# Kernel tuning notes

Measured on AMD Instinct MI355X. Metric: run time of the kernel, lower is better.

The kernel has to match this reference:

```python
import jax, jax.numpy as jnp
import numpy as np

# Fixed architecture constants (from DMGHAN.__init__ / Mamba defaults)
D_MODEL = 256; D_STATE = 16; D_CONV = 4; D_INNER = 512; DT_RANK = 16
EMBED = 1024; N_CLASSES = [5, 30, 80, 200, 600, 1500]
B, L = 8, 2048


def setup_inputs() -> dict:
    key = jax.random.key(0)
    ks = jax.random.split(key, 32)
    def p(i, shape, s=0.02):
        return jax.random.normal(ks[i], shape, jnp.float32) * s
    inp = {
        "x": jax.random.normal(ks[0], (B, L, EMBED), jnp.float32),
        # input_proj
        "W_proj": p(1, (D_MODEL, EMBED)), "b_proj": p(2, (D_MODEL,)),
        # Mamba block params
        "W_in": p(3, (2 * D_INNER, D_MODEL)),
        "conv_w": p(4, (D_INNER, 1, D_CONV), 0.1), "conv_b": p(5, (D_INNER,), 0.1),
        "W_xp": p(6, (DT_RANK + 2 * D_STATE, D_INNER)),
        "W_dt": p(7, (D_INNER, DT_RANK), 0.1), "b_dt": p(8, (D_INNER,), 0.1),
        "A_log": jnp.log(jnp.broadcast_to(jnp.arange(1., D_STATE + 1., dtype=jnp.float32), (D_INNER, D_STATE))),
        "Dp": jnp.ones((D_INNER,), jnp.float32),
        "W_out": p(9, (D_MODEL, D_INNER)),
        # 6 MultiheadAttention layers (in_proj packed [q;k;v], out_proj)
        "mha_in_w": p(10, (6, 3 * D_MODEL, D_MODEL)), "mha_in_b": p(11, (6, 3 * D_MODEL)),
        "mha_out_w": p(12, (6, D_MODEL, D_MODEL)), "mha_out_b": p(13, (6, D_MODEL)),
        # 5 gates: Linear(512, 256) + sigmoid
        "gate_w": p(14, (5, D_MODEL, 2 * D_MODEL)), "gate_b": p(15, (5, D_MODEL)),
    }
    for i, nc in enumerate(N_CLASSES):
        inp[f"Wc{i}"] = p(16 + i, (nc, D_MODEL))
        inp[f"bc{i}"] = p(22 + i, (nc,))
    return inp


def mamba_block(x, W_in, conv_w, conv_b, W_xp, W_dt, b_dt, A_log, Dp, W_out):
    # x: (B, L, D_MODEL)
    u, z = jnp.split(x @ W_in.T, 2, axis=-1)          # each (B, L, D_INNER)
    # causal depthwise conv over time
    uc = jax.lax.conv_general_dilated(
        u.transpose(0, 2, 1), conv_w, window_strides=(1,),
        padding=[(D_CONV - 1, 0)], dimension_numbers=('NCH', 'OIH', 'NCH'),
        feature_group_count=D_INNER)
    u = jax.nn.silu(uc.transpose(0, 2, 1) + conv_b)    # (B, L, D_INNER)
    xdbc = u @ W_xp.T                                  # (B, L, DT_RANK + 2*N)
    dt = jax.nn.softplus(xdbc[..., :DT_RANK] @ W_dt.T + b_dt)   # (B, L, D_INNER)
    Bm = xdbc[..., DT_RANK:DT_RANK + D_STATE]          # (B, L, N)
    Cm = xdbc[..., DT_RANK + D_STATE:]                 # (B, L, N)
    A = -jnp.exp(A_log)                                # (D_INNER, N)

    def step(h, inp):
        d_t, B_t, C_t, u_t = inp                       # (B,D_INNER),(B,N),(B,N),(B,D_INNER)
        h = jnp.exp(d_t[..., None] * A) * h + (d_t * u_t)[..., None] * B_t[:, None, :]
        y = jnp.einsum('bdn,bn->bd', h, C_t)
        return h, y

    h0 = jnp.zeros((x.shape[0], D_INNER, D_STATE), x.dtype)
    xs = (dt.transpose(1, 0, 2), Bm.transpose(1, 0, 2), Cm.transpose(1, 0, 2), u.transpose(1, 0, 2))
    _, ys = jax.lax.scan(step, h0, xs)                 # ys: (L, B, D_INNER)
    y = ys.transpose(1, 0, 2) + u * Dp
    y = y * jax.nn.silu(z)
    return y @ W_out.T                                 # (B, L, D_MODEL)


def reference(x, W_proj, b_proj, W_in, conv_w, conv_b, W_xp, W_dt, b_dt, A_log, Dp, W_out,
              mha_in_w, mha_in_b, mha_out_w, mha_out_b, gate_w, gate_b,
              Wc0, bc0, Wc1, bc1, Wc2, bc2, Wc3, bc3, Wc4, bc4, Wc5, bc5):
    h = x @ W_proj.T + b_proj                          # (B, L, 256)
    seq = mamba_block(h, W_in, conv_w, conv_b, W_xp, W_dt, b_dt, A_log, Dp, W_out)
    pooled = seq.mean(axis=1)                          # (B, 256)

    feats = []
    cur = None
    for i in range(6):
        if i == 0:
            f = pooled
        else:
            g = jax.nn.sigmoid(jnp.concatenate([cur, pooled], -1) @ gate_w[i - 1].T + gate_b[i - 1])
            f = g * cur + (1. - g) * pooled
        # MHA self-attention with seq_len=1: softmax over a single key is identically 1,
        # so attn_out = out_proj(v_proj(f)) exactly (same value AND gradients).
        v = f @ mha_in_w[i][2 * D_MODEL:].T + mha_in_b[i][2 * D_MODEL:]
        cur = v @ mha_out_w[i].T + mha_out_b[i]
        feats.append(cur)

    Wcs = [Wc0, Wc1, Wc2, Wc3, Wc4, Wc5]
    bcs = [bc0, bc1, bc2, bc3, bc4, bc5]
    return tuple(f @ W.T + b for f, W, b in zip(feats, Wcs, bcs))
```

## Files before the change

kernel.cpp:

```cpp
#include <hip/hip_runtime.h>
#include <stdint.h>

typedef unsigned short u16;
typedef uint32_t u32;
typedef __attribute__((ext_vector_type(8))) short bf16x8;
typedef __attribute__((ext_vector_type(4))) float f32x4;

__device__ __forceinline__ float bf2f(u16 u){ return __uint_as_float(((u32)u) << 16); }
__device__ __forceinline__ u16 f2bf(float f){
    u32 u = __float_as_uint(f);
    u += 0x7FFFu + ((u >> 16) & 1u);
    return (u16)(u >> 16);
}

#define AS1(p) ((const __attribute__((address_space(1))) void*)(p))
#define AS3(p) ((__attribute__((address_space(3))) void*)(p))

#define HW_GATE 0
#define HW_WVT  655360
#define HW_WO   1048576
#define HW_WOV  1441792
#define HW_TOT  1835008

#define NBLK 16
#define NC   64
#define CT   32

__global__ __launch_bounds__(256)
void convert_x(const float* __restrict__ xsrc, u16* __restrict__ dst)
{
    const int i = (blockIdx.x*256 + threadIdx.x)*8;
    const float4 a = *(const float4*)(xsrc + i);
    const float4 b = *(const float4*)(xsrc + i + 4);
    ushort4 o0; o0.x=f2bf(a.x); o0.y=f2bf(a.y); o0.z=f2bf(a.z); o0.w=f2bf(a.w);
    ushort4 o1; o1.x=f2bf(b.x); o1.y=f2bf(b.y); o1.z=f2bf(b.z); o1.w=f2bf(b.w);
    *(ushort4*)(dst+i) = o0; *(ushort4*)(dst+i+4) = o1;
}

__global__ __launch_bounds__(256)
void convert_w(const float* __restrict__ W_proj, const float* __restrict__ W_in,
               const float* __restrict__ W_xp,  const float* __restrict__ gate_w,
               const float* __restrict__ mha_in_w, const float* __restrict__ mha_out_w,
               u16* __restrict__ wproj, u16* __restrict__ win,
               u16* __restrict__ wxpp,  u16* __restrict__ whead,
               float* __restrict__ ysumG, unsigned* __restrict__ cnt)
{
    const int gid = blockIdx.x*256 + threadIdx.x;
    if(gid < 262144){
        wproj[gid] = f2bf(W_proj[gid]);
    } else if(gid < 786432){
        const int g = gid - 262144;
        win[g] = f2bf(W_in[g]);
    } else if(gid < 851968){
        const int g = gid - 786432;
        wxpp[g] = ((g >> 9) < 48) ? f2bf(W_xp[g]) : (u16)0;
    } else if(gid < 1507328){
        const int g = gid - 851968;
        whead[HW_GATE + g] = f2bf(gate_w[g]);
    } else if(gid < 1900544){
        const int g = gid - 1507328;
        const int i = g >> 16, k = (g >> 8) & 255, j = g & 255;
        whead[HW_WVT + g] = f2bf(mha_in_w[(size_t)i*196608 + 131072 + (size_t)j*256 + k]);
    } else if(gid < 2293760){
        const int g = gid - 1900544;
        whead[HW_WO + g] = f2bf(mha_out_w[g]);
    } else if(gid < 2297856){
        ysumG[gid - 2293760] = 0.f;
    } else if(gid < 2297920){
        cnt[gid - 2297856] = 0u;
    }
}

template<int EPI>
__global__ __launch_bounds__(256)
void gemm_bt(const u16* __restrict__ A, const u16* __restrict__ B,
             const float* __restrict__ bias, u16* __restrict__ C,
             int K, int lda, int ldb, int ldc, int nTilesN)
{
    __shared__ __align__(16) u16 As[128*32];
    __shared__ __align__(16) u16 Bs[128*32];
    const int tid  = threadIdx.x;
    const int nwg  = gridDim.x;
    const int bid0 = blockIdx.x;
    const int bid  = ((nwg & 7) == 0) ? (bid0 & 7)*(nwg >> 3) + (bid0 >> 3) : bid0;
    const int bm   = bid / nTilesN, bn = bid % nTilesN;
    const int m0   = bm*128, n0 = bn*128;
    const int lane = tid & 63, wave = tid >> 6;
    const int r1 = tid >> 2,        p1 = tid & 3;
    const int r2 = (tid+256) >> 2,  p2 = (tid+256) & 3;
    const u16* gA1 = A + (size_t)(m0 + r1)*lda + p1*8;
    const u16* gA2 = A + (size_t)(m0 + r2)*lda + p2*8;
    const u16* gB1 = B + (size_t)(n0 + r1)*ldb + p1*8;
    const u16* gB2 = B + (size_t)(n0 + r2)*ldb + p2*8;
    u16* lA1 = As + wave*512;
    u16* lA2 = As + 2048 + wave*512;
    u16* lB1 = Bs + wave*512;
    u16* lB2 = Bs + 2048 + wave*512;

    f32x4 acc[4][4];
    #pragma unroll
    for(int i=0;i<4;i++)
        #pragma unroll
        for(int j=0;j<4;j++) acc[i][j] = (f32x4){0.f,0.f,0.f,0.f};

    const int wm = (wave>>1)*64, wn = (wave&1)*64;
    const int fr = lane & 15, fq = lane >> 4;

    for(int k0 = 0; k0 < K; k0 += 32){
        __syncthreads();
        __builtin_amdgcn_global_load_lds(AS1(gA1 + k0), AS3(lA1), 16, 0, 0);
        __builtin_amdgcn_global_load_lds(AS1(gA2 + k0), AS3(lA2), 16, 0, 0);
        __builtin_amdgcn_global_load_lds(AS1(gB1 + k0), AS3(lB1), 16, 0, 0);
        __builtin_amdgcn_global_load_lds(AS1(gB2 + k0), AS3(lB2), 16, 0, 0);
        __syncthreads();
        bf16x8 af[4], bw[4];
        #pragma unroll
        for(int i=0;i<4;i++){
            af[i] = *(const bf16x8*)(As + (wm + 16*i + fr)*32 + fq*8);
            bw[i] = *(const bf16x8*)(Bs + (wn + 16*i + fr)*32 + fq*8);
        }
        #pragma unroll
        for(int i=0;i<4;i++)
            #pragma unroll
            for(int j=0;j<4;j++)
                acc[i][j] = __builtin_amdgcn_mfma_f32_16x16x32_bf16(af[i], bw[j], acc[i][j], 0,0,0);
    }

    const int mbase = m0 + wm + fq*4;
    #pragma unroll
    for(int j=0;j<4;j++){
        const int ncol = n0 + wn + 16*j + fr;
        const float bv = (EPI >= 1) ? bias[ncol] : 0.f;
        #pragma unroll
        for(int i=0;i<4;i++){
            #pragma unroll
            for(int r=0;r<4;r++){
                C[(size_t)(mbase + 16*i + r)*ldc + ncol] = f2bf(acc[i][j][r] + bv);
            }
        }
    }
}

__global__ __launch_bounds__(256)
void wov_k(u16* __restrict__ whead)
{
    __shared__ __align__(16) u16 As[128*32];
    __shared__ __align__(16) u16 Bs[128*32];
    const int tid  = threadIdx.x;
    const int st   = blockIdx.x >> 2;
    const int tile = blockIdx.x & 3;
    const int m0   = (tile>>1)*128, n0 = (tile&1)*128;
    const u16* A = whead + HW_WO  + (size_t)st*65536;
    const u16* B = whead + HW_WVT + (size_t)st*65536;
    u16*       C = whead + HW_WOV + (size_t)st*65536;
    const int lane = tid & 63, wave = tid >> 6;
    const int r1 = tid >> 2,        p1 = tid & 3;
    const int r2 = (tid+256) >> 2,  p2 = (tid+256) & 3;
    const u16* gA1 = A + (size_t)(m0 + r1)*256 + p1*8;
    const u16* gA2 = A + (size_t)(m0 + r2)*256 + p2*8;
    const u16* gB1 = B + (size_t)(n0 + r1)*256 + p1*8;
    const u16* gB2 = B + (size_t)(n0 + r2)*256 + p2*8;
    u16* lA1 = As + wave*512;
    u16* lA2 = As + 2048 + wave*512;
    u16* lB1 = Bs + wave*512;
    u16* lB2 = Bs + 2048 + wave*512;

    f32x4 acc[4][4];
    #pragma unroll
    for(int i=0;i<4;i++)
        #pragma unroll
        for(int j=0;j<4;j++) acc[i][j] = (f32x4){0.f,0.f,0.f,0.f};

    const int wm = (wave>>1)*64, wn = (wave&1)*64;
    const int fr = lane & 15, fq = lane >> 4;

    for(int k0 = 0; k0 < 256; k0 += 32){
        __syncthreads();
        __builtin_amdgcn_global_load_lds(AS1(gA1 + k0), AS3(lA1), 16, 0, 0);
        __builtin_amdgcn_global_load_lds(AS1(gA2 + k0), AS3(lA2), 16, 0, 0);
        __builtin_amdgcn_global_load_lds(AS1(gB1 + k0), AS3(lB1), 16, 0, 0);
        __builtin_amdgcn_global_load_lds(AS1(gB2 + k0), AS3(lB2), 16, 0, 0);
        __syncthreads();
        bf16x8 af[4], bw[4];
        #pragma unroll
        for(int i=0;i<4;i++){
            af[i] = *(const bf16x8*)(As + (wm + 16*i + fr)*32 + fq*8);
            bw[i] = *(const bf16x8*)(Bs + (wn + 16*i + fr)*32 + fq*8);
        }
        #pragma unroll
        for(int i=0;i<4;i++)
            #pragma unroll
            for(int j=0;j<4;j++)
                acc[i][j] = __builtin_amdgcn_mfma_f32_16x16x32_bf16(af[i], bw[j], acc[i][j], 0,0,0);
    }

    const int mbase = m0 + wm + fq*4;
    #pragma unroll
    for(int j=0;j<4;j++){
        const int ncol = n0 + wn + 16*j + fr;
        #pragma unroll
        for(int i=0;i<4;i++){
            #pragma unroll
            for(int r=0;r<4;r++){
                C[(size_t)(mbase + 16*i + r)*256 + ncol] = f2bf(acc[i][j][r]);
            }
        }
    }
}

__global__ __launch_bounds__(256)
void bcomb_k(const float* __restrict__ mha_out_w, const float* __restrict__ mha_in_b,
             const float* __restrict__ mha_out_b, float* __restrict__ bcomb)
{
    const int st = blockIdx.x, n = threadIdx.x;
    __shared__ float bv[256];
    bv[n] = mha_in_b[st*768 + 512 + n];
    __syncthreads();
    const float* w = mha_out_w + (size_t)st*65536 + (size_t)n*256;
    float s = mha_out_b[st*256 + n];
    for(int k=0;k<256;k++) s += w[k]*bv[k];
    bcomb[st*256 + n] = s;
}

__global__ __launch_bounds__(256)
void dt_kernel(const u16* __restrict__ xdbc, const float* __restrict__ W_dt,
               const float* __restrict__ b_dt, u16* __restrict__ dtb)
{
    const int m0 = blockIdx.x*64;
    const int d0 = threadIdx.x;
    float w0[16], w1[16];
    #pragma unroll
    for(int k=0;k<16;k++){ w0[k]=W_dt[d0*16+k]; w1[k]=W_dt[(d0+256)*16+k]; }
    const float bb0=b_dt[d0], bb1=b_dt[d0+256];
    for(int r=0;r<64;r++){
        const int m=m0+r;
        const bf16x8 v0 = *(const bf16x8*)(xdbc + (size_t)m*128);
        const bf16x8 v1 = *(const bf16x8*)(xdbc + (size_t)m*128 + 8);
        float a0=bb0, a1=bb1;
        #pragma unroll
        for(int k=0;k<8;k++){ const float xv=bf2f((u16)v0[k]); a0+=xv*w0[k]; a1+=xv*w1[k]; }
        #pragma unroll
        for(int k=0;k<8;k++){ const float xv=bf2f((u16)v1[k]); a0+=xv*w0[k+8]; a1+=xv*w1[k+8]; }
        a0 = (a0>15.f)? a0 : __logf(1.f+__expf(a0));
        a1 = (a1>15.f)? a1 : __logf(1.f+__expf(a1));
        dtb[(size_t)m*512+d0]     = f2bf(a0);
        dtb[(size_t)m*512+d0+256] = f2bf(a1);
    }
}

__global__ __launch_bounds__(256)
void conv_silu(const u16* __restrict__ xin, const float* __restrict__ conv_w,
               const float* __restrict__ conv_b, u16* __restrict__ u2)
{
    const int idx = blockIdx.x*256 + threadIdx.x;
    const int d = idx & 511;
    const int m = idx >> 9;
    const int l = m & 2047;
    const u16* base = xin + (size_t)m*1024 + d;
    float acc = conv_b[d];
    const float w0 = conv_w[d*4+0];
    const float w1 = conv_w[d*4+1];
    const float w2 = conv_w[d*4+2];
    const float w3 = conv_w[d*4+3];
    if(l >= 3) acc += bf2f(base[-3*1024])*w0;
    if(l >= 2) acc += bf2f(base[-2*1024])*w1;
    if(l >= 1) acc += bf2f(base[-1*1024])*w2;
    acc += bf2f(base[0])*w3;
    u2[idx] = f2bf(acc / (1.f + __expf(-acc)));
}

__global__ __launch_bounds__(512)
void scan_a(const u16* __restrict__ dtb, const u16* __restrict__ u2,
            const u16* __restrict__ xdbc,
            float* __restrict__ dts_out, float* __restrict__ S)
{
    const int b = blockIdx.x >> 6, c = blockIdx.x & 63;
    const int d = threadIdx.x;
    const int m0 = b*2048 + c*CT;
    __shared__ float Bsh[CT][16];
    {
        const int tt = d >> 4, n = d & 15;
        Bsh[tt][n] = bf2f(xdbc[(size_t)(m0+tt)*128 + 16 + n]);
    }
    __syncthreads();
    float h[16];
    #pragma unroll
    for(int n=0;n<16;n++) h[n] = 0.f;
    float dts = 0.f;
    for(int tb=0; tb<CT; tb+=8){
        float dtv[8], uv[8];
        #pragma unroll
        for(int q=0;q<8;q++){
            const size_t m = (size_t)(m0+tb+q)*512 + d;
            dtv[q] = bf2f(dtb[m]);
            uv[q]  = bf2f(u2[m]);
        }
        #pragma unroll
        for(int q=0;q<8;q++){
            const float du = dtv[q]*uv[q];
            dts += dtv[q];
            const float r = __expf(-dtv[q]);
            float p = 1.f;
            #pragma unroll
            for(int n=0;n<16;n++){
                p *= r;
                h[n] = p*h[n] + du*Bsh[tb+q][n];
            }
        }
    }
    const size_t o = (size_t)(b*NC + c)*512 + d;
    dts_out[o] = dts;
    #pragma unroll
    for(int n=0;n<16;n++) S[o*16 + n] = h[n];
}

__global__ __launch_bounds__(256)
void scan_b(const float* __restrict__ dts, float* __restrict__ S )
{
    const int gid = blockIdx.x*256 + threadIdx.x;
    const int b = gid >> 13;
    const int dn = gid & 8191;
    const int d = dn >> 4;
    const float nf = (float)((dn & 15) + 1);
    float h = 0.f;
    for(int c=0;c<NC;c++){
        const size_t od = (size_t)(b*NC + c)*512 + d;
        const float pn = __expf(-nf * dts[od]);
        const size_t o = od*16 + (dn & 15);
        const float s = S[o];
        S[o] = h;
        h = pn*h + s;
    }
}

__global__ __launch_bounds__(512)
void scan_c(const u16* __restrict__ dtb, const u16* __restrict__ u2,
            const u16* __restrict__ xdbc, const u16* __restrict__ xin,
            const float* __restrict__ Dp, const float* __restrict__ Hin,
            float* __restrict__ ysumG)
{
    const int b = blockIdx.x >> 6, c = blockIdx.x & 63;
    const int d = threadIdx.x;
    const int m0 = b*2048 + c*CT;
    __shared__ float Bsh[CT][16];
    __shared__ float Csh[CT][16];
    {
        const int tt = d >> 4, n = d & 15;
        const size_t row = (size_t)(m0+tt)*128;
        Bsh[tt][n] = bf2f(xdbc[row + 16 + n]);
        Csh[tt][n] = bf2f(xdbc[row + 32 + n]);
    }
    __syncthreads();
    const float Dpd = Dp[d];
    const size_t ho = ((size_t)(b*NC + c)*512 + d)*16;
    float h[16];
    #pragma unroll
    for(int n=0;n<16;n++) h[n] = Hin[ho+n];
    float ysum = 0.f;
    for(int tb=0; tb<CT; tb+=8){
        float dtv[8], uv[8], zv[8];
        #pragma unroll
        for(int q=0;q<8;q++){
            const size_t m = (size_t)(m0+tb+q)*512 + d;
            dtv[q] = bf2f(dtb[m]);
            uv[q]  = bf2f(u2[m]);
            zv[q]  = bf2f(xin[(size_t)(m0+tb+q)*1024 + 512 + d]);
        }
        #pragma unroll
        for(int q=0;q<8;q++){
            const float du = dtv[q]*uv[q];
            const float r = __expf(-dtv[q]);
            float p = 1.f;
            float y = 0.f;
            #pragma unroll
            for(int n=0;n<16;n++){
                p *= r;
                h[n] = p*h[n] + du*Bsh[tb+q][n];
                y += h[n]*Csh[tb+q][n];
            }
            y += uv[q]*Dpd;
            y *= zv[q] / (1.f + __expf(-zv[q]));
            ysum += y;
        }
    }
    atomicAdd(&ysumG[b*512 + d], ysum);
}

__device__ __forceinline__ void gridbar(unsigned* cnt, int ep)
{
    __syncthreads();
    if(threadIdx.x == 0){
        __threadfence();
        __hip_atomic_fetch_add(cnt, 1u, __ATOMIC_RELEASE, __HIP_MEMORY_SCOPE_AGENT);
        const unsigned tgt = (unsigned)(NBLK*ep);
        while(__hip_atomic_load(cnt, __ATOMIC_RELAXED, __HIP_MEMORY_SCOPE_AGENT) < tgt)
            __builtin_amdgcn_s_sleep(2);
        __threadfence();
    }
    __syncthreads();
}

__global__ __launch_bounds__(256)
void head_coop(const float* __restrict__ ysumG, const float* __restrict__ W_out,
               const u16* __restrict__ whead, const float* __restrict__ bcomb,
               const float* __restrict__ gate_b,
               u16* __restrict__ plA, u16* __restrict__ clA, u16* __restrict__ vA,
               float* __restrict__ feats, unsigned* cnt)
{
    __shared__ float pscr[2048];
    __shared__ float plL[128], clL[128];
    __shared__ float PgL[768];
    const int tid  = threadIdx.x;
    const int nb0  = blockIdx.x*16;
    const int lane = tid & 63, wave = tid >> 6;
    const int fr = lane & 15, fq = lane >> 4;
    const int nn = nb0 + fr;
    int ep = 0;

    {
        const int col16 = tid >> 4, seg = tid & 15;
        float part[8];
        #pragma unroll
        for(int b=0;b<8;b++) part[b] = 0.f;
        const float* wrow = W_out + (size_t)(nb0 + col16)*512 + seg*32;
        const float* ys   = ysumG + seg*32;
        for(int dd=0; dd<32; dd++){
            const float w = wrow[dd];
            #pragma unroll
            for(int b=0;b<8;b++) part[b] += ys[b*512 + dd]*w;
        }
        #pragma unroll
        for(int b=0;b<8;b++) pscr[(seg*16 + col16)*8 + b] = part[b];
        __syncthreads();
        if(tid < 128){
            const int b = tid & 7, c16 = tid >> 3;
            float s = 0.f;
            for(int g=0; g<16; g++) s += pscr[(g*16 + c16)*8 + b];
            s *= (1.f/2048.f);
            plL[b*16 + c16] = s;
            plA[b*256 + nb0 + c16] = f2bf(s);
        } else {
            const int idx = tid - 128, r = 8 + (idx >> 4), c = idx & 15;
            const int off = r*256 + nb0 + c;
            plA[off] = 0; clA[off] = 0; vA[off] = 0;
        }
    }
    gridbar(cnt, ++ep);

    if(wave == 0){
        bf16x8 af[8];
        #pragma unroll
        for(int i=0;i<8;i++) af[i] = *(const bf16x8*)(plA + fr*256 + i*32 + fq*8);
        {
            const u16* wb = whead + HW_WOV + (size_t)nn*256 + fq*8;
            bf16x8 bw[8];
            #pragma unroll
            for(int i=0;i<8;i++) bw[i] = *(const bf16x8*)(wb + i*32);
            f32x4 acc = (f32x4){0.f,0.f,0.f,0.f};
            #pragma unroll
            for(int i=0;i<8;i++)
                acc = __builtin_amdgcn_mfma_f32_16x16x32_bf16(af[i], bw[i], acc, 0,0,0);
            const float bc = bcomb[nn];
            #pragma unroll
            for(int r=0;r<4;r++){
                const int bi = fq*4 + r;
                if(bi < 8){
                    const float cv = acc[r] + bc;
                    clL[bi*16 + fr] = cv;
                    clA[bi*256 + nn] = f2bf(cv);
                    feats[bi*256 + nn] = cv;
                }
            }
        }
        #pragma unroll
        for(int st=1; st<6; st++){
            const u16* wb = whead + HW_GATE + (size_t)(st-1)*131072
                          + (size_t)nn*512 + 256 + fq*8;
            bf16x8 bw[8];
            #pragma unroll
            for(int i=0;i<8;i++) bw[i] = *(const bf16x8*)(wb + i*32);
            f32x4 acc = (f32x4){0.f,0.f,0.f,0.f};
            #pragma unroll
            for(int i=0;i<8;i++)
                acc = __builtin_amdgcn_mfma_f32_16x16x32_bf16(af[i], bw[i], acc, 0,0,0);
            const float gb = gate_b[(st-1)*256 + nn];
            #pragma unroll
            for(int r=0;r<4;r++){
                const int bi = fq*4 + r;
                if(bi < 8) PgL[st*128 + bi*16 + fr] = acc[r] + gb;
            }
        }
    }
    gridbar(cnt, ++ep);

    for(int st=1; st<6; st++){
        if(wave == 0){
            const u16* wb = whead + HW_GATE + (size_t)(st-1)*131072
                          + (size_t)nn*512 + fq*8;
            bf16x8 af[8], bw[8];
            #pragma unroll
            for(int i=0;i<8;i++) bw[i] = *(const bf16x8*)(wb + i*32);
            #pragma unroll
            for(int i=0;i<8;i++) af[i] = *(const bf16x8*)(clA + fr*256 + i*32 + fq*8);
            f32x4 acc = (f32x4){0.f,0.f,0.f,0.f};
            #pragma unroll
            for(int i=0;i<8;i++)
                acc = __builtin_amdgcn_mfma_f32_16x16x32_bf16(af[i], bw[i], acc, 0,0,0);
            #pragma unroll
            for(int r=0;r<4;r++){
                const int bi = fq*4 + r;
                if(bi < 8){
                    const float t = acc[r] + PgL[st*128 + bi*16 + fr];
                    const float g = 1.f/(1.f + __expf(-t));
                    const float f = g*clL[bi*16 + fr] + (1.f - g)*plL[bi*16 + fr];
                    vA[bi*256 + nn] = f2bf(f);
                }
            }
        }
        gridbar(cnt, ++ep);
        if(wave == 0){
            const u16* wb = whead + HW_WOV + (size_t)st*65536 + (size_t)nn*256 + fq*8;
            bf16x8 af[8], bw[8];
            #pragma unroll
            for(int i=0;i<8;i++) bw[i] = *(const bf16x8*)(wb + i*32);
            #pragma unroll
            for(int i=0;i<8;i++) af[i] = *(const bf16x8*)(vA + fr*256 + i*32 + fq*8);
            f32x4 acc = (f32x4){0.f,0.f,0.f,0.f};
            #pragma unroll
            for(int i=0;i<8;i++)
                acc = __builtin_amdgcn_mfma_f32_16x16x32_bf16(af[i], bw[i], acc, 0,0,0);
            const float bc = bcomb[st*256 + nn];
            #pragma unroll
            for(int r=0;r<4;r++){
                const int bi = fq*4 + r;
                if(bi < 8){
                    const float cv = acc[r] + bc;
                    clL[bi*16 + fr] = cv;
                    clA[bi*256 + nn] = f2bf(cv);
                    feats[(size_t)st*2048 + bi*256 + nn] = cv;
                }
            }
        }
        if(st < 5) gridbar(cnt, ++ep);
    }
}

__global__ __launch_bounds__(256)
void classifier_k(const float* __restrict__ feats,
    const float* __restrict__ W0, const float* __restrict__ b0,
    const float* __restrict__ W1, const float* __restrict__ b1,
    const float* __restrict__ W2, const float* __restrict__ b2,
    const float* __restrict__ W3, const float* __restrict__ b3,
    const float* __restrict__ W4, const float* __restrict__ b4,
    const float* __restrict__ W5, const float* __restrict__ b5,
    float* __restrict__ out)
{
    const int tid = blockIdx.x*256 + threadIdx.x;
    if(tid >= 19320) return;
    const int b  = tid & 7;
    const int ic = tid >> 3;
    int i, c, nc, ooff;
    const float *W, *bb;
    if(ic < 5)       { i=0; c=ic;      nc=5;    ooff=0;    W=W0; bb=b0; }
    else if(ic<35)   { i=1; c=ic-5;    nc=30;   ooff=40;   W=W1; bb=b1; }
    else if(ic<115)  { i=2; c=ic-35;   nc=80;   ooff=280;  W=W2; bb=b2; }
    else if(ic<315)  { i=3; c=ic-115;  nc=200;  ooff=920;  W=W3; bb=b3; }
    else if(ic<915)  { i=4; c=ic-315;  nc=600;  ooff=2520; W=W4; bb=b4; }
    else             { i=5; c=ic-915;  nc=1500; ooff=7320; W=W5; bb=b5; }
    const float4* f4 = (const float4*)(feats + ((size_t)i*8 + b)*256);
    const float4* w4 = (const float4*)(W + (size_t)c*256);
    float acc = bb[c];
    #pragma unroll 8
    for(int m=0;m<64;m++){
        const float4 a = f4[m], w = w4[m];
        acc += a.x*w.x + a.y*w.y + a.z*w.z + a.w*w.w;
    }
    out[ooff + b*nc + c] = acc;
}

extern "C" void kernel_launch(void* const* d_in, const int* in_sizes, int n_in,
                              void* d_out, int out_size, void* d_ws, size_t ws_size,
                              hipStream_t stream)
{
    const float* x         = (const float*)d_in[0];
    const float* W_proj    = (const float*)d_in[1];
    const float* b_proj    = (const float*)d_in[2];
    const float* W_in      = (const float*)d_in[3];
    const float* conv_w    = (const float*)d_in[4];
    const float* conv_b    = (const float*)d_in[5];
    const float* W_xp      = (const float*)d_in[6];
    const float* W_dt      = (const float*)d_in[7];
    const float* b_dt      = (const float*)d_in[8];
    const float* Dp        = (const float*)d_in[10];
    const float* W_out     = (const float*)d_in[11];
    const float* mha_in_w  = (const float*)d_in[12];
    const float* mha_in_b  = (const float*)d_in[13];
    const float* mha_out_w = (const float*)d_in[14];
    const float* mha_out_b = (const float*)d_in[15];
    const float* gate_w    = (const float*)d_in[16];
    const float* gate_b    = (const float*)d_in[17];

    char* ws = (char*)d_ws;
    u16*   xbf    = (u16*)  (ws + 0);
    u16*   xin    = (u16*)  (ws + 0);
    u16*   h      = (u16*)  (ws + 33554432);
    float* dts    = (float*)(ws + 33554432);
    u16*   u2     = (u16*)  (ws + 41943040);
    u16*   xdbc   = (u16*)  (ws + 58720256);
    u16*   dtb    = (u16*)  (ws + 62914560);
    float* S      = (float*)(ws + 79691776);
    float* ysumG  = (float*)(ws + 96468992);
    unsigned* cnt = (unsigned*)(ws + 96468992 + 16384);
    u16*   plA    = (u16*)  (ws + 96468992 + 16640);
    u16*   clA    = (u16*)  (ws + 96468992 + 24832);
    u16*   vA     = (u16*)  (ws + 96468992 + 33024);
    float* feats  = (float*)(ws + 97001472);
    u16*   wproj  = (u16*)  (ws + 97058816);
    u16*   win    = (u16*)  (ws + 97583104);
    u16*   wxpp   = (u16*)  (ws + 98631680);
    u16*   whead  = (u16*)  (ws + 98762752);
    float* bcomb  = (float*)(ws + 102432768);

    convert_x<<<dim3(8192), 256, 0, stream>>>(x, xbf);
    convert_w<<<dim3(8977), 256, 0, stream>>>(W_proj, W_in, W_xp, gate_w,
                                              mha_in_w, mha_out_w,
                                              wproj, win, wxpp, whead,
                                              ysumG, cnt);
    wov_k<<<dim3(24), 256, 0, stream>>>(whead);
    bcomb_k<<<dim3(6), 256, 0, stream>>>(mha_out_w, mha_in_b, mha_out_b, bcomb);

    gemm_bt<1><<<dim3(128*2), 256, 0, stream>>>(xbf, wproj, b_proj, h,
        1024, 1024, 1024, 256, 2);
    gemm_bt<0><<<dim3(128*8), 256, 0, stream>>>(h, win, nullptr, xin,
        256, 256, 256, 1024, 8);
    conv_silu<<<dim3(32768), 256, 0, stream>>>(xin, conv_w, conv_b, u2);
    gemm_bt<0><<<dim3(128), 256, 0, stream>>>(u2, wxpp, nullptr, xdbc,
        512, 512, 512, 128, 1);
    dt_kernel<<<dim3(256), 256, 0, stream>>>(xdbc, W_dt, b_dt, dtb);

    scan_a<<<dim3(512), 512, 0, stream>>>(dtb, u2, xdbc, dts, S);
    scan_b<<<dim3(256), 256, 0, stream>>>(dts, S);
    scan_c<<<dim3(512), 512, 0, stream>>>(dtb, u2, xdbc, xin, Dp, S, ysumG);

    head_coop<<<dim3(NBLK), 256, 0, stream>>>(ysumG, W_out, whead, bcomb,
                                              gate_b, plA, clA, vA, feats, cnt);

    classifier_k<<<dim3(76), 256, 0, stream>>>(feats,
        (const float*)d_in[18], (const float*)d_in[19],
        (const float*)d_in[20], (const float*)d_in[21],
        (const float*)d_in[22], (const float*)d_in[23],
        (const float*)d_in[24], (const float*)d_in[25],
        (const float*)d_in[26], (const float*)d_in[27],
        (const float*)d_in[28], (const float*)d_in[29],
        (float*)d_out);
}
```

Measured before the change: 439.1 us.

## Fold gate weights into value/out projections to halve grid barriers in head

```diff
diff --git a/kernel.cpp b/kernel.cpp
--- a/kernel.cpp
+++ b/kernel.cpp
@@ -21,6 +21,7 @@
 #define HW_WO   1048576
 #define HW_WOV  1441792
 #define HW_TOT  1835008
+#define HW_WGV  HW_WVT
 
 #define NBLK 16
 #define NC   64
@@ -209,6 +210,144 @@
 }
 
 __global__ __launch_bounds__(256)
+void wovT_k(const u16* __restrict__ whead, u16* __restrict__ wovt)
+{
+    __shared__ __align__(16) u16 As[128*32];
+    __shared__ __align__(16) u16 Bs[128*32];
+    const int tid  = threadIdx.x;
+    const int st   = blockIdx.x >> 2;
+    const int tile = blockIdx.x & 3;
+    const int m0   = (tile>>1)*128, n0 = (tile&1)*128;
+    const u16* A = whead + HW_WVT + (size_t)st*65536;
+    const u16* B = whead + HW_WO  + (size_t)st*65536;
+    u16*       C = wovt + (size_t)st*65536;
+    const int lane = tid & 63, wave = tid >> 6;
+    const int r1 = tid >> 2,        p1 = tid & 3;
+    const int r2 = (tid+256) >> 2,  p2 = (tid+256) & 3;
+    const u16* gA1 = A + (size_t)(m0 + r1)*256 + p1*8;
+    const u16* gA2 = A + (size_t)(m0 + r2)*256 + p2*8;
+    const u16* gB1 = B + (size_t)(n0 + r1)*256 + p1*8;
+    const u16* gB2 = B + (size_t)(n0 + r2)*256 + p2*8;
+    u16* lA1 = As + wave*512;
+    u16* lA2 = As + 2048 + wave*512;
+    u16* lB1 = Bs + wave*512;
+    u16* lB2 = Bs + 2048 + wave*512;
+
+    f32x4 acc[4][4];
+    #pragma unroll
+    for(int i=0;i<4;i++)
+        #pragma unroll
+        for(int j=0;j<4;j++) acc[i][j] = (f32x4){0.f,0.f,0.f,0.f};
+
+    const int wm = (wave>>1)*64, wn = (wave&1)*64;
+    const int fr = lane & 15, fq = lane >> 4;
+
+    for(int k0 = 0; k0 < 256; k0 += 32){
+        __syncthreads();
+        __builtin_amdgcn_global_load_lds(AS1(gA1 + k0), AS3(lA1), 16, 0, 0);
+        __builtin_amdgcn_global_load_lds(AS1(gA2 + k0), AS3(lA2), 16, 0, 0);
+        __builtin_amdgcn_global_load_lds(AS1(gB1 + k0), AS3(lB1), 16, 0, 0);
+        __builtin_amdgcn_global_load_lds(AS1(gB2 + k0), AS3(lB2), 16, 0, 0);
+        __syncthreads();
+        bf16x8 af[4], bw[4];
+        #pragma unroll
+        for(int i=0;i<4;i++){
+            af[i] = *(const bf16x8*)(As + (wm + 16*i + fr)*32 + fq*8);
+            bw[i] = *(const bf16x8*)(Bs + (wn + 16*i + fr)*32 + fq*8);
+        }
+        #pragma unroll
+        for(int i=0;i<4;i++)
+            #pragma unroll
+            for(int j=0;j<4;j++)
+                acc[i][j] = __builtin_amdgcn_mfma_f32_16x16x32_bf16(af[i], bw[j], acc[i][j], 0,0,0);
+    }
+
+    const int mbase = m0 + wm + fq*4;
+    #pragma unroll
+    for(int j=0;j<4;j++){
+        const int ncol = n0 + wn + 16*j + fr;
+        #pragma unroll
+        for(int i=0;i<4;i++){
+            #pragma unroll
+            for(int r=0;r<4;r++){
+                C[(size_t)(mbase + 16*i + r)*256 + ncol] = f2bf(acc[i][j][r]);
+            }
+        }
+    }
+}
+
+__global__ __launch_bounds__(256)
+void wgv_k(u16* __restrict__ whead, const u16* __restrict__ wovt)
+{
+    __shared__ __align__(16) u16 As[128*32];
+    __shared__ __align__(16) u16 Bs[128*32];
+    const int tid  = threadIdx.x;
+    const int st1  = blockIdx.x >> 2;
+    const int tile = blockIdx.x & 3;
+    const int m0   = (tile>>1)*128, n0 = (tile&1)*128;
+    const u16* A = whead + HW_GATE + (size_t)st1*131072;
+    const u16* B = wovt + (size_t)st1*65536;
+    u16*       C = whead + HW_WGV + (size_t)st1*65536;
+    const int lane = tid & 63, wave = tid >> 6;
+    const int r1 = tid >> 2,        p1 = tid & 3;
+    const int r2 = (tid+256) >> 2,  p2 = (tid+256) & 3;
+    const u16* gA1 = A + (size_t)(m0 + r1)*512 + p1*8;
+    const u16* gA2 = A + (size_t)(m0 + r2)*512 + p2*8;
+    const u16* gB1 = B + (size_t)(n0 + r1)*256 + p1*8;
+    const u16* gB2 = B + (size_t)(n0 + r2)*256 + p2*8;
+    u16* lA1 = As + wave*512;
+    u16* lA2 = As + 2048 + wave*512;
+    u16* lB1 = Bs + wave*512;
+    u16* lB2 = Bs + 2048 + wave*512;
+
+    f32x4 acc[4][4];
+    #pragma unroll
+    for(int i=0;i<4;i++)
+        #pragma unroll
+        for(int j=0;j<4;j++) acc[i][j] = (f32x4){0.f,0.f,0.f,0.f};
+
+    const int wm = (wave>>1)*64, wn = (wave&1)*64;
+    const int fr = lane & 15, fq = lane >> 4;
+
+    for(int k0 = 0; k0 < 256; k0 += 32){
+        __syncthreads();
+        __builtin_amdgcn_global_load_lds(AS1(gA1 + k0), AS3(lA1), 16, 0, 0);
+        __builtin_amdgcn_global_load_lds(AS1(gA2 + k0), AS3(lA2), 16, 0, 0);
+        __builtin_amdgcn_global_load_lds(AS1(gB1 + k0), AS3(lB1), 16, 0, 0);
+        __builtin_amdgcn_global_load_lds(AS1(gB2 + k0), AS3(lB2), 16, 0, 0);
+        __syncthreads();
+        bf16x8 af[4], bw[4];
+        #pragma unroll
+        for(int i=0;i<4;i++){
+            af[i] = *(const bf16x8*)(As + (wm + 16*i + fr)*32 + fq*8);
+            bw[i] = *(const bf16x8*)(Bs + (wn + 16*i + fr)*32 + fq*8);
+        }
+        #pragma unroll
+        for(int i=0;i<4;i++)
+            #pragma unroll
+            for(int j=0;j<4;j++)
+                acc[i][j] = __builtin_amdgcn_mfma_f32_16x16x32_bf16(af[i], bw[j], acc[i][j], 0,0,0);
+    }
+
+    const int mbase = m0 + wm + fq*4;
+    #pragma unroll
+    for(int j=0;j<4;j++){
+        const int ncol = n0 + wn + 16*j + fr;
+        #pragma unroll
+        for(int i=0;i<4;i++){
+            #pragma unroll
+            for(int r=0;r<4;r++){
+                const int mrow = mbase + 16*i + r;
+                float v = acc[i][j][r];
+                if(st1 == 0)
+                    v += bf2f(whead[HW_GATE + (size_t)mrow*512 + 256 + ncol]);
+                C[(size_t)mrow*256 + ncol] = f2bf(v);
+            }
+        }
+    }
+}
+
+__global__ __launch_bounds__(256)
 void bcomb_k(const float* __restrict__ mha_out_w, const float* __restrict__ mha_in_b,
              const float* __restrict__ mha_out_b, float* __restrict__ bcomb)
 {
@@ -220,6 +359,20 @@
     float s = mha_out_b[st*256 + n];
     for(int k=0;k<256;k++) s += w[k]*bv[k];
     bcomb[st*256 + n] = s;
+}
+
+__global__ __launch_bounds__(256)
+void bfold_k(const u16* __restrict__ whead, const float* __restrict__ bcomb,
+             const float* __restrict__ gate_b, float* __restrict__ bq)
+{
+    const int st1 = blockIdx.x, j = threadIdx.x;
+    __shared__ float bc[256];
+    bc[j] = bcomb[st1*256 + j];
+    __syncthreads();
+    const u16* w = whead + HW_GATE + (size_t)st1*131072 + (size_t)j*512;
+    float s = gate_b[st1*256 + j];
+    for(int k=0;k<256;k++) s += bc[k]*bf2f(w[k]);
+    bq[st1*256 + j] = s;
 }
 
 __global__ __launch_bounds__(256)
@@ -403,12 +556,12 @@
 __global__ __launch_bounds__(256)
 void head_coop(const float* __restrict__ ysumG, const float* __restrict__ W_out,
                const u16* __restrict__ whead, const float* __restrict__ bcomb,
-               const float* __restrict__ gate_b,
-               u16* __restrict__ plA, u16* __restrict__ clA, u16* __restrict__ vA,
+               const float* __restrict__ bq,
+               u16* __restrict__ plA, u16* __restrict__ fA0, u16* __restrict__ fA1,
                float* __restrict__ feats, unsigned* cnt)
 {
     __shared__ float pscr[2048];
-    __shared__ float plL[128], clL[128];
+    __shared__ float plL[128];
     __shared__ float PgL[768];
     const int tid  = threadIdx.x;
     const int nb0  = blockIdx.x*16;
@@ -442,7 +595,7 @@
         } else {
             const int idx = tid - 128, r = 8 + (idx >> 4), c = idx & 15;
             const int off = r*256 + nb0 + c;
-            plA[off] = 0; clA[off] = 0; vA[off] = 0;
+            plA[off] = 0; fA0[off] = 0; fA1[off] = 0;
         }
     }
     gridbar(cnt, ++ep);
@@ -451,97 +604,115 @@
         bf16x8 af[8];
         #pragma unroll
         for(int i=0;i<8;i++) af[i] = *(const bf16x8*)(plA + fr*256 + i*32 + fq*8);
+        f32x4 acc0 = (f32x4){0.f,0.f,0.f,0.f};
         {
             const u16* wb = whead + HW_WOV + (size_t)nn*256 + fq*8;
-            bf16x8 bw[8];
-            #pragma unroll
-            for(int i=0;i<8;i++) bw[i] = *(const bf16x8*)(wb + i*32);
+            #pragma unroll
+            for(int i=0;i<8;i++){
+                const bf16x8 bw = *(const bf16x8*)(wb + i*32);
+                acc0 = __builtin_amdgcn_mfma_f32_16x16x32_bf16(af[i], bw, acc0, 0,0,0);
+            }
+        }
+        f32x4 acc1 = (f32x4){0.f,0.f,0.f,0.f};
+        {
+            const u16* wb = whead + HW_WGV + (size_t)nn*256 + fq*8;
+            #pragma unroll
+            for(int i=0;i<8;i++){
+                const bf16x8 bw = *(const bf16x8*)(wb + i*32);
+                acc1 = __builtin_amdgcn_mfma_f32_16x16x32_bf16(af[i], bw, acc1, 0,0,0);
+            }
+        }
+        const float bc0 = bcomb[nn], bq1 = bq[nn];
+        #pragma unroll
+        for(int r=0;r<4;r++){
+            const int bi = fq*4 + r;
+            if(bi < 8){
+                const float cv = acc0[r] + bc0;
+                feats[bi*256 + nn] = cv;
+                const float g = 1.f/(1.f + __expf(-(acc1[r] + bq1)));
+                const float f = g*cv + (1.f - g)*plL[bi*16 + fr];
+                fA1[bi*256 + nn] = f2bf(f);
+            }
+        }
+        #pragma unroll
+        for(int st=2; st<6; st++){
+            const u16* wb = whead + HW_GATE + (size_t)(st-1)*131072
+                          + (size_t)nn*512 + 256 + fq*8;
             f32x4 acc = (f32x4){0.f,0.f,0.f,0.f};
             #pragma unroll
-            for(int i=0;i<8;i++)
-                acc = __builtin_amdgcn_mfma_f32_16x16x32_bf16(af[i], bw[i], acc, 0,0,0);
-            const float bc = bcomb[nn];
+            for(int i=0;i<8;i++){
+                const bf16x8 bw = *(const bf16x8*)(wb + i*32);
+                acc = __builtin_amdgcn_mfma_f32_16x16x32_bf16(af[i], bw, acc, 0,0,0);
+            }
+            #pragma unroll
+            for(int r=0;r<4;r++){
+                const int bi = fq*4 + r;
+                if(bi < 8) PgL[st*128 + bi*16 + fr] = acc[r];
+            }
+        }
+    }
+    gridbar(cnt, ++ep);
+
+    for(int st=2; st<6; st++){
+        if(wave == 0){
+            const u16* fsrc = ((st-1) & 1) ? fA1 : fA0;
+            u16*       fdst = (st & 1) ? fA1 : fA0;
+            bf16x8 af[8];
+            #pragma unroll
+            for(int i=0;i<8;i++) af[i] = *(const bf16x8*)(fsrc + fr*256 + i*32 + fq*8);
+            f32x4 acc0 = (f32x4){0.f,0.f,0.f,0.f};
+            {
+                const u16* wb = whead + HW_WOV + (size_t)(st-1)*65536 + (size_t)nn*256 + fq*8;
+                #pragma unroll
+                for(int i=0;i<8;i++){
+                    const bf16x8 bw = *(const bf16x8*)(wb + i*32);
+                    acc0 = __builtin_amdgcn_mfma_f32_16x16x32_bf16(af[i], bw, acc0, 0,0,0);
+                }
+            }
+            f32x4 acc1 = (f32x4){0.f,0.f,0.f,0.f};
+            {
+                const u16* wb = whead + HW_WGV + (size_t)(st-1)*65536 + (size_t)nn*256 + fq*8;
+                #pragma unroll
+                for(int i=0;i<8;i++){
+                    const bf16x8 bw = *(const bf16x8*)(wb + i*32);
+                    acc1 = __builtin_amdgcn_mfma_f32_16x16x32_bf16(af[i], bw, acc1, 0,0,0);
+                }
+            }
+            const float bc = bcomb[(st-1)*256 + nn];
+            const float bqv = bq[(st-1)*256 + nn];
             #pragma unroll
             for(int r=0;r<4;r++){
                 const int bi = fq*4 + r;
                 if(bi < 8){
-                    const float cv = acc[r] + bc;
-                    clL[bi*16 + fr] = cv;
-                    clA[bi*256 + nn] = f2bf(cv);
-                    feats[bi*256 + nn] = cv;
+                    const float cv = acc0[r] + bc;
+                    feats[(size_t)(st-1)*2048 + bi*256 + nn] = cv;
+                    const float t = acc1[r] + PgL[st*128 + bi*16 + fr] + bqv;
+                    const float g = 1.f/(1.f + __expf(-t));
+                    const float f = g*cv + (1.f - g)*plL[bi*16 + fr];
+                    fdst[bi*256 + nn] = f2bf(f);
                 }
             }
         }
-        #pragma unroll
-        for(int st=1; st<6; st++){
-            const u16* wb = whead + HW_GATE + (size_t)(st-1)*131072
-                          + (size_t)nn*512 + 256 + fq*8;
-            bf16x8 bw[8];
-            #pragma unroll
-            for(int i=0;i<8;i++) bw[i] = *(const bf16x8*)(wb + i*32);
-            f32x4 acc = (f32x4){0.f,0.f,0.f,0.f};
-            #pragma unroll
-            for(int i=0;i<8;i++)
-                acc = __builtin_amdgcn_mfma_f32_16x16x32_bf16(af[i], bw[i], acc, 0,0,0);
-            const float gb = gate_b[(st-1)*256 + nn];
-            #pragma unroll
-            for(int r=0;r<4;r++){
-                const int bi = fq*4 + r;
-                if(bi < 8) PgL[st*128 + bi*16 + fr] = acc[r] + gb;
-            }
-        }
-    }
-    gridbar(cnt, ++ep);
-
-    for(int st=1; st<6; st++){
-        if(wave == 0){
-            const u16* wb = whead + HW_GATE + (size_t)(st-1)*131072
-                          + (size_t)nn*512 + fq*8;
-            bf16x8 af[8], bw[8];
-            #pragma unroll
-            for(int i=0;i<8;i++) bw[i] = *(const bf16x8*)(wb + i*32);
-            #pragma unroll
-            for(int i=0;i<8;i++) af[i] = *(const bf16x8*)(clA + fr*256 + i*32 + fq*8);
-            f32x4 acc = (f32x4){0.f,0.f,0.f,0.f};
-            #pragma unroll
-            for(int i=0;i<8;i++)
-                acc = __builtin_amdgcn_mfma_f32_16x16x32_bf16(af[i], bw[i], acc, 0,0,0);
-            #pragma unroll
-            for(int r=0;r<4;r++){
-                const int bi = fq*4 + r;
-                if(bi < 8){
-                    const float t = acc[r] + PgL[st*128 + bi*16 + fr];
-                    const float g = 1.f/(1.f + __expf(-t));
-                    const float f = g*clL[bi*16 + fr] + (1.f - g)*plL[bi*16 + fr];
-                    vA[bi*256 + nn] = f2bf(f);
-                }
-            }
-        }
         gridbar(cnt, ++ep);
-        if(wave == 0){
-            const u16* wb = whead + HW_WOV + (size_t)st*65536 + (size_t)nn*256 + fq*8;
-            bf16x8 af[8], bw[8];
-            #pragma unroll
-            for(int i=0;i<8;i++) bw[i] = *(const bf16x8*)(wb + i*32);
-            #pragma unroll
-            for(int i=0;i<8;i++) af[i] = *(const bf16x8*)(vA + fr*256 + i*32 + fq*8);
-            f32x4 acc = (f32x4){0.f,0.f,0.f,0.f};
-            #pragma unroll
-            for(int i=0;i<8;i++)
-                acc = __builtin_amdgcn_mfma_f32_16x16x32_bf16(af[i], bw[i], acc, 0,0,0);
-            const float bc = bcomb[st*256 + nn];
-            #pragma unroll
-            for(int r=0;r<4;r++){
-                const int bi = fq*4 + r;
-                if(bi < 8){
-                    const float cv = acc[r] + bc;
-                    clL[bi*16 + fr] = cv;
-                    clA[bi*256 + nn] = f2bf(cv);
-                    feats[(size_t)st*2048 + bi*256 + nn] = cv;
-                }
-            }
-        }
-        if(st < 5) gridbar(cnt, ++ep);
+    }
+
+    if(wave == 0){
+        bf16x8 af[8];
+        #pragma unroll
+        for(int i=0;i<8;i++) af[i] = *(const bf16x8*)(fA1 + fr*256 + i*32 + fq*8);
+        f32x4 acc0 = (f32x4){0.f,0.f,0.f,0.f};
+        const u16* wb = whead + HW_WOV + (size_t)5*65536 + (size_t)nn*256 + fq*8;
+        #pragma unroll
+        for(int i=0;i<8;i++){
+            const bf16x8 bw = *(const bf16x8*)(wb + i*32);
+            acc0 = __builtin_amdgcn_mfma_f32_16x16x32_bf16(af[i], bw, acc0, 0,0,0);
+        }
+        const float bc = bcomb[5*256 + nn];
+        #pragma unroll
+        for(int r=0;r<4;r++){
+            const int bi = fq*4 + r;
+            if(bi < 8) feats[(size_t)5*2048 + bi*256 + nn] = acc0[r] + bc;
+        }
     }
 }
 
@@ -608,18 +779,20 @@
     u16*   u2     = (u16*)  (ws + 41943040);
     u16*   xdbc   = (u16*)  (ws + 58720256);
     u16*   dtb    = (u16*)  (ws + 62914560);
+    u16*   wovt   = (u16*)  (ws + 62914560);
     float* S      = (float*)(ws + 79691776);
     float* ysumG  = (float*)(ws + 96468992);
     unsigned* cnt = (unsigned*)(ws + 96468992 + 16384);
     u16*   plA    = (u16*)  (ws + 96468992 + 16640);
-    u16*   clA    = (u16*)  (ws + 96468992 + 24832);
-    u16*   vA     = (u16*)  (ws + 96468992 + 33024);
+    u16*   fA0    = (u16*)  (ws + 96468992 + 24832);
+    u16*   fA1    = (u16*)  (ws + 96468992 + 33024);
     float* feats  = (float*)(ws + 97001472);
     u16*   wproj  = (u16*)  (ws + 97058816);
     u16*   win    = (u16*)  (ws + 97583104);
     u16*   wxpp   = (u16*)  (ws + 98631680);
     u16*   whead  = (u16*)  (ws + 98762752);
     float* bcomb  = (float*)(ws + 102432768);
+    float* bq     = (float*)(ws + 102438912);
 
     convert_x<<<dim3(8192), 256, 0, stream>>>(x, xbf);
     convert_w<<<dim3(8977), 256, 0, stream>>>(W_proj, W_in, W_xp, gate_w,
@@ -627,7 +800,10 @@
                                               wproj, win, wxpp, whead,
                                               ysumG, cnt);
     wov_k<<<dim3(24), 256, 0, stream>>>(whead);
+    wovT_k<<<dim3(20), 256, 0, stream>>>(whead, wovt);
+    wgv_k<<<dim3(20), 256, 0, stream>>>(whead, wovt);
     bcomb_k<<<dim3(6), 256, 0, stream>>>(mha_out_w, mha_in_b, mha_out_b, bcomb);
+    bfold_k<<<dim3(5), 256, 0, stream>>>(whead, bcomb, gate_b, bq);
 
     gemm_bt<1><<<dim3(128*2), 256, 0, stream>>>(xbf, wproj, b_proj, h,
         1024, 1024, 1024, 256, 2);
@@ -642,8 +818,8 @@
     scan_b<<<dim3(256), 256, 0, stream>>>(dts, S);
     scan_c<<<dim3(512), 512, 0, stream>>>(dtb, u2, xdbc, xin, Dp, S, ysumG);
 
-    head_coop<<<dim3(NBLK), 256, 0, stream>>>(ysumG, W_out, whead, bcomb,
-                                              gate_b, plA, clA, vA, feats, cnt);
+    head_coop<<<dim3(NBLK), 256, 0, stream>>>(ysumG, W_out, whead, bcomb, bq,
+                                              plA, fA0, fA1, feats, cnt);
 
     classifier_k<<<dim3(76), 256, 0, stream>>>(feats,
         (const float*)d_in[18], (const float*)d_in[19],
```

Result: slower. 455.1 us (+3.6%).
